# Optimization experiments

Hardware: AMD Instinct MI355X
Metric: run time of the kernel (lower is better)

## Reference

```python
import jax, jax.numpy as jnp
import numpy as np

BATCH, SEQ = 2, 4096
IN_FEATURES = 4096
OUT_FEATURES = 4096
BLOCK = 64                      # oft_block_size (bs)
RANK = IN_FEATURES // BLOCK     # number of diagonal blocks (r)


def setup_inputs() -> dict:
    key = jax.random.key(0)
    k1, k2, k3, k4 = jax.random.split(key, 4)
    x = jax.random.normal(k1, (BATCH, SEQ, IN_FEATURES), dtype=jnp.float32)
    # OFT adapter parameters: one (bs x bs) generator per block
    oft_r = jax.random.normal(k2, (RANK, BLOCK, BLOCK), dtype=jnp.float32) * 0.02
    # Dequantized GPTQ weight (out_features x in_features) + bias
    W = jax.random.normal(k3, (OUT_FEATURES, IN_FEATURES), dtype=jnp.float32) * 0.02
    b = jax.random.normal(k4, (OUT_FEATURES,), dtype=jnp.float32)
    return {"x": x, "oft_r": oft_r, "W": W, "b": b}


def _cayley_batch(data):
    # data: [r, bs, bs].  Q = (I - skew) @ (I + skew)^{-1}  (torch.linalg.solve left=False)
    bs = data.shape[-1]
    skew = 0.5 * (data - jnp.swapaxes(data, -1, -2))
    I = jnp.eye(bs, dtype=data.dtype)
    A = I + skew   # [r, bs, bs]
    B = I - skew
    # Solve Q A = B  ->  A^T Q^T = B^T
    Qt = jnp.linalg.solve(jnp.swapaxes(A, -1, -2), jnp.swapaxes(B, -1, -2))
    return jnp.swapaxes(Qt, -1, -2)


def reference(x, oft_r, W, b):
    rank, bs, _ = oft_r.shape
    # oft_rotation starts as identity; single active adapter -> rotation = Cayley(oft_r)
    oft_rotation = _cayley_batch(oft_r)            # [rank, bs, bs]
    batch_dims = x.shape[:-1]
    x_reshaped = x.reshape(*batch_dims, rank, bs)  # [..., r, k]
    x_rot = jnp.einsum('...rk,rkc->...rc', x_reshaped, oft_rotation)
    x_rot = x_rot.reshape(*batch_dims, rank * bs)  # [..., in_features]
    # quant_linear_module (dequantized): y = x_rot @ W^T + b
    return jnp.einsum('bsi,oi->bso', x_rot, W) + b
```

## Files before the change

kernel.cpp:

```cpp
#include <hip/hip_runtime.h>
#include <hip/hip_bf16.h>
#include <stdint.h>


typedef __bf16 bf16;
typedef __attribute__((ext_vector_type(4))) __bf16 bf16x4;
typedef __attribute__((ext_vector_type(8))) __bf16 bf16x8;
typedef __attribute__((ext_vector_type(4))) float f32x4;

__device__ __forceinline__ bf16 f2bf(float f) {
  unsigned u = __builtin_bit_cast(unsigned, f);
  u += 0x7fffu + ((u >> 16) & 1u);
  unsigned short h = (unsigned short)(u >> 16);
  return __builtin_bit_cast(bf16, h);
}

__global__ __launch_bounds__(256) void cayley_kernel(const float* __restrict__ oft_r,
                                                     float* __restrict__ Qxt) {
  __shared__ float St[64][68];
  __shared__ float Ta[64][65];
  __shared__ float Tb[64][65];
  const int tid = threadIdx.x;
  const int r = blockIdx.x;
  const float* D = oft_r + (size_t)r * 4096;

  for (int idx = tid; idx < 4096; idx += 256) {
    int i = idx >> 6, j = idx & 63;
    float s = 0.5f * (D[i * 64 + j] - D[j * 64 + i]);
    St[j][i] = s;
    Ta[i][j] = (i == j ? 1.0f : 0.0f) - s;
  }
  __syncthreads();

  const int j = tid & 63;
  const int w = tid >> 6;
  float (*Tin)[65] = Ta;
  float (*Tout)[65] = Tb;

  for (int it = 0; it < 5; ++it) {
    float out[16];
#pragma unroll
    for (int m = 0; m < 16; ++m) out[m] = ((w * 16 + m) == j ? 1.0f : 0.0f);
    for (int c = 0; c < 64; ++c) {
      float tc = Tin[c][j];
      f32x4 s0 = *reinterpret_cast<const f32x4*>(&St[c][w * 16]);
      f32x4 s1 = *reinterpret_cast<const f32x4*>(&St[c][w * 16 + 4]);
      f32x4 s2 = *reinterpret_cast<const f32x4*>(&St[c][w * 16 + 8]);
      f32x4 s3 = *reinterpret_cast<const f32x4*>(&St[c][w * 16 + 12]);
#pragma unroll
      for (int q = 0; q < 4; ++q) {
        out[q]      -= s0[q] * tc;
        out[4 + q]  -= s1[q] * tc;
        out[8 + q]  -= s2[q] * tc;
        out[12 + q] -= s3[q] * tc;
      }
    }
#pragma unroll
    for (int m = 0; m < 16; ++m) Tout[w * 16 + m][j] = out[m];
    __syncthreads();
    float (*tmp)[65] = Tin; Tin = Tout; Tout = tmp;
  }
  {
    float out[16];
#pragma unroll
    for (int m = 0; m < 16; ++m) out[m] = Tin[w * 16 + m][j];
    for (int c = 0; c < 64; ++c) {
      float tc = Tin[c][j];
      f32x4 s0 = *reinterpret_cast<const f32x4*>(&St[c][w * 16]);
      f32x4 s1 = *reinterpret_cast<const f32x4*>(&St[c][w * 16 + 4]);
      f32x4 s2 = *reinterpret_cast<const f32x4*>(&St[c][w * 16 + 8]);
      f32x4 s3 = *reinterpret_cast<const f32x4*>(&St[c][w * 16 + 12]);
#pragma unroll
      for (int q = 0; q < 4; ++q) {
        out[q]      -= s0[q] * tc;
        out[4 + q]  -= s1[q] * tc;
        out[8 + q]  -= s2[q] * tc;
        out[12 + q] -= s3[q] * tc;
      }
    }
#pragma unroll
    for (int m = 0; m < 16; ++m) Qxt[(size_t)r * 4096 + (w * 16 + m) * 64 + j] = out[m];
  }
}

__global__ __launch_bounds__(256) void foldcast_kernel(const float* __restrict__ W,
                                                       const float* __restrict__ Qxt,
                                                       bf16* __restrict__ Wp,
                                                       const float* __restrict__ x,
                                                       bf16* __restrict__ xb, long n) {
  __shared__ bf16 Wb[128 * 64];
  __shared__ bf16 Xt[64 * 64];
  const int tid = threadIdx.x;

  if (blockIdx.x >= 2048) {
    long i0 = ((long)(blockIdx.x - 2048) * 256 + tid) * 8;
    long stride = (long)(gridDim.x - 2048) * 256 * 8;
    for (long i = i0; i < n; i += stride) {
      f32x4 a = *reinterpret_cast<const f32x4*>(x + i);
      f32x4 b = *reinterpret_cast<const f32x4*>(x + i + 4);
      bf16x8 o;
      o[0] = f2bf(a[0]); o[1] = f2bf(a[1]); o[2] = f2bf(a[2]); o[3] = f2bf(a[3]);
      o[4] = f2bf(b[0]); o[5] = f2bf(b[1]); o[6] = f2bf(b[2]); o[7] = f2bf(b[3]);
      *reinterpret_cast<bf16x8*>(xb + i) = o;
    }
    return;
  }

  const int lane = tid & 63;
  const int wave = tid >> 6;
  const int o0 = (blockIdx.x & 31) * 128;
  const int r = blockIdx.x >> 5;
  const int fr = lane & 15;
  const int kg = lane >> 4;

#pragma unroll
  for (int i = 0; i < 8; ++i) {
    int c = i * 256 + tid;
    int row = c >> 4, c4 = c & 15;
    f32x4 v = *reinterpret_cast<const f32x4*>(W + (size_t)(o0 + row) * 4096 + r * 64 + c4 * 4);
    bf16x4 o; o[0] = f2bf(v[0]); o[1] = f2bf(v[1]); o[2] = f2bf(v[2]); o[3] = f2bf(v[3]);
    *reinterpret_cast<bf16x4*>(&Wb[row * 64 + c4 * 4]) = o;
  }
#pragma unroll
  for (int i = 0; i < 4; ++i) {
    int c = i * 256 + tid;
    int row = c >> 4, c4 = c & 15;
    f32x4 v = *reinterpret_cast<const f32x4*>(Qxt + (size_t)r * 4096 + row * 64 + c4 * 4);
    bf16x4 o; o[0] = f2bf(v[0]); o[1] = f2bf(v[1]); o[2] = f2bf(v[2]); o[3] = f2bf(v[3]);
    *reinterpret_cast<bf16x4*>(&Xt[row * 64 + c4 * 4]) = o;
  }
  __syncthreads();

  const int wm = wave * 32;
  f32x4 acc[2][4];
#pragma unroll
  for (int mi = 0; mi < 2; ++mi)
#pragma unroll
    for (int ni = 0; ni < 4; ++ni) acc[mi][ni] = (f32x4){0.f, 0.f, 0.f, 0.f};

#pragma unroll
  for (int kk = 0; kk < 64; kk += 32) {
    bf16x8 af[2], bx[4];
#pragma unroll
    for (int mi = 0; mi < 2; ++mi)
      af[mi] = *reinterpret_cast<const bf16x8*>(&Wb[(wm + mi * 16 + fr) * 64 + kk + kg * 8]);
#pragma unroll
    for (int ni = 0; ni < 4; ++ni)
      bx[ni] = *reinterpret_cast<const bf16x8*>(&Xt[(ni * 16 + fr) * 64 + kk + kg * 8]);
#pragma unroll
    for (int mi = 0; mi < 2; ++mi)
#pragma unroll
      for (int ni = 0; ni < 4; ++ni)
        acc[mi][ni] = __builtin_amdgcn_mfma_f32_16x16x32_bf16(af[mi], bx[ni], acc[mi][ni], 0, 0, 0);
  }

#pragma unroll
  for (int mi = 0; mi < 2; ++mi)
#pragma unroll
    for (int ni = 0; ni < 4; ++ni)
#pragma unroll
      for (int q = 0; q < 4; ++q) {
        int row = o0 + wm + mi * 16 + kg * 4 + q;
        int col = ni * 16 + fr;
        Wp[(size_t)row * 4096 + r * 64 + col] = f2bf(acc[mi][ni][q]);
      }
}


#define GLDS16(g, l) __builtin_amdgcn_global_load_lds( \
    (const __attribute__((address_space(1))) unsigned int*)(g), \
    (__attribute__((address_space(3))) unsigned int*)(l), 16, 0, 0)

#define VMCNT12 asm volatile("s_waitcnt vmcnt(12)" ::: "memory")
#define VMCNT8  asm volatile("s_waitcnt vmcnt(8)" ::: "memory")
#define VMCNT4  asm volatile("s_waitcnt vmcnt(4)" ::: "memory")
#define VMCNT0  asm volatile("s_waitcnt vmcnt(0)" ::: "memory")
#define NOWAIT  do {} while (0)
#define BARRIER() do { asm volatile("" ::: "memory"); \
  __builtin_amdgcn_s_barrier(); asm volatile("" ::: "memory"); } while (0)

#define MFMA16(AF, BF, RB) \
  _Pragma("unroll") \
  for (int m_ = 0; m_ < 4; ++m_) \
    _Pragma("unroll") \
    for (int n_ = 0; n_ < 4; ++n_) \
      acc[RB + m_][n_] = __builtin_amdgcn_mfma_f32_16x16x32_bf16(AF[m_], BF[n_], acc[RB + m_][n_], 0, 0, 0);

#define DO_T(S0, S1, SA, SB, TN, PRE, W2, W1) do { \
     \
    _Pragma("unroll") for (int n_ = 0; n_ < 4; ++n_) Ob[n_] = LDB(S0, n_); \
    _Pragma("unroll") for (int m_ = 0; m_ < 4; ++m_) Oa[m_] = LDA(S0, m_); \
    if (PRE) STG_A(TN, SA, 0); \
    BARRIER(); \
    __builtin_amdgcn_s_setprio(1); MFMA16(Oa, Ob, 0) __builtin_amdgcn_s_setprio(0); \
     \
    _Pragma("unroll") for (int m_ = 0; m_ < 4; ++m_) Ea[m_] = LDA(S0, 4 + m_); \
    if (PRE) STG_B(TN, SA, 0); \
    W2; \
    BARRIER(); \
    __builtin_amdgcn_s_setprio(1); MFMA16(Ea, Ob, 4) __builtin_amdgcn_s_setprio(0); \
     \
    _Pragma("unroll") for (int n_ = 0; n_ < 4; ++n_) Eb[n_] = LDB(S1, n_); \
    _Pragma("unroll") for (int m_ = 0; m_ < 4; ++m_) Oa[m_] = LDA(S1, m_); \
    if (PRE) STG_A(TN, SB, 1); \
    BARRIER(); \
    __builtin_amdgcn_s_setprio(1); MFMA16(Oa, Eb, 0) __builtin_amdgcn_s_setprio(0); \
     \
    _Pragma("unroll") for (int m_ = 0; m_ < 4; ++m_) Ea[m_] = LDA(S1, 4 + m_); \
    if (PRE) STG_B(TN, SB, 1); \
    W1; \
    BARRIER(); \
    __builtin_amdgcn_s_setprio(1); MFMA16(Ea, Eb, 4) __builtin_amdgcn_s_setprio(0); \
  } while (0)

__global__ __launch_bounds__(512, 2) void gemm_kernel(const bf16* __restrict__ A,
                                                      const bf16* __restrict__ B,
                                                      const float* __restrict__ bias,
                                                      float* __restrict__ C,
                                                      int M, int N, int K) {
  __shared__ bf16 lds[81920];
  const int tid = threadIdx.x;
  const int lane = tid & 63;
  const int wave = tid >> 6;
  const int wr = wave >> 2;
  const int wc = wave & 3;
  const int fr = lane & 15;
  const int kg = lane >> 4;
  const int m0 = blockIdx.y * 256;
  const int n0 = blockIdx.x * 256;

  f32x4 acc[8][4];
#pragma unroll
  for (int m = 0; m < 8; ++m)
#pragma unroll
    for (int n = 0; n < 4; ++n) acc[m][n] = (f32x4){0.f, 0.f, 0.f, 0.f};

  auto STG = [&](const bf16* src, int base_row, int t, int ks, int ldsbase) {
#pragma unroll
    for (int i = 0; i < 2; ++i) {
      int c = i * 512 + tid;
      int row = c >> 2, cc = c & 3;
      const bf16* g = src + (size_t)(base_row + row) * K + t * 64 + ks * 32
                      + ((cc ^ ((row >> 1) & 3)) << 3);
      GLDS16(g, &lds[ldsbase + ((i * 512 + wave * 64) << 3)]);
    }
  };
  auto STG_A = [&](int t, int slot, int ks) { STG(A, m0, t, ks, slot * 16384); };
  auto STG_B = [&](int t, int slot, int ks) { STG(B, n0, t, ks, slot * 16384 + 8192); };

  auto LDA = [&](int slot, int mi) -> bf16x8 {
    int row = wr * 128 + mi * 16 + fr;
    return *reinterpret_cast<const bf16x8*>(
        &lds[slot * 16384 + row * 32 + ((kg ^ ((row >> 1) & 3)) << 3)]);
  };
  auto LDB = [&](int slot, int ni) -> bf16x8 {
    int row = wc * 64 + ni * 16 + fr;
    return *reinterpret_cast<const bf16x8*>(
        &lds[slot * 16384 + 8192 + row * 32 + ((kg ^ ((row >> 1) & 3)) << 3)]);
  };

  STG_A(0, 0, 0); STG_B(0, 0, 0); STG_A(0, 1, 1); STG_B(0, 1, 1);
  STG_A(1, 2, 0); STG_B(1, 2, 0); STG_A(1, 3, 1); STG_B(1, 3, 1);
  VMCNT12;
  BARRIER();

  bf16x8 Oa[4], Ob[4], Ea[4], Eb[4];
  for (int t = 0; t < 60; t += 5) {
    DO_T(0, 1, 4, 0, t + 2, true, VMCNT12, VMCNT12);
    DO_T(2, 3, 1, 2, t + 3, true, VMCNT12, VMCNT12);
    DO_T(4, 0, 3, 4, t + 4, true, VMCNT12, VMCNT12);
    DO_T(1, 2, 0, 1, t + 5, true, VMCNT12, VMCNT12);
    DO_T(3, 4, 2, 3, t + 6, true, VMCNT12, VMCNT12);
  }
  DO_T(0, 1, 4, 0, 62, true,  VMCNT12, VMCNT12);
  DO_T(2, 3, 1, 2, 63, true,  VMCNT12, VMCNT12);
  DO_T(4, 0, 0, 0, 0,  false, VMCNT8,  VMCNT4);
  DO_T(1, 2, 0, 0, 0,  false, VMCNT0,  NOWAIT);

#pragma unroll
  for (int n = 0; n < 4; ++n) {
    int col = n0 + wc * 64 + n * 16 + fr;
    float bv = bias[col];
#pragma unroll
    for (int m = 0; m < 8; ++m) {
      int row0 = m0 + wr * 128 + m * 16 + kg * 4;
#pragma unroll
      for (int q = 0; q < 4; ++q)
        C[(size_t)(row0 + q) * N + col] = acc[m][n][q] + bv;
    }
  }
}

extern "C" void kernel_launch(void* const* d_in, const int* in_sizes, int n_in,
                              void* d_out, int out_size, void* d_ws, size_t ws_size,
                              hipStream_t stream) {
  const float* x     = (const float*)d_in[0];
  const float* oft_r = (const float*)d_in[1];
  const float* W     = (const float*)d_in[2];
  const float* b     = (const float*)d_in[3];
  float* y = (float*)d_out;

  char* ws = (char*)d_ws;
  float* Qxt = (float*)ws;
  bf16*  Wp  = (bf16*)(ws + (1u << 20));
  bf16*  xb  = (bf16*)(ws + (1u << 20) + (32u << 20));

  cayley_kernel<<<64, 256, 0, stream>>>(oft_r, Qxt);
  foldcast_kernel<<<4096, 256, 0, stream>>>(W, Qxt, Wp, x, xb, 33554432L);
  dim3 gg(4096 / 256, 8192 / 256);
  gemm_kernel<<<gg, 512, 0, stream>>>(xb, Wp, b, y, 8192, 4096, 4096);
}
```

Before: 323.0 us.

## Fuse Cayley solve and weight folding into one prep kernel

Merges the Cayley-transform kernel and the fold/cast kernel into one launch. Each of the first 64 blocks computes its rotation block in shared memory and keeps it in LDS as bf16, then loops over all 32 output chunks of W to fold it in. The remaining blocks cast x to bf16 at the same time. This removes a kernel launch and the fp32 Qxt round trip through global memory, and lets the x cast overlap the Cayley iterations. In exchange, all W folding is serialized onto only 64 blocks, each looping 32 times with barriers, which risks a long tail.

```diff
diff --git a/kernel.cpp b/kernel.cpp
--- a/kernel.cpp
+++ b/kernel.cpp
@@ -15,12 +15,34 @@
   return __builtin_bit_cast(bf16, h);
 }
 
-__global__ __launch_bounds__(256) void cayley_kernel(const float* __restrict__ oft_r,
-                                                     float* __restrict__ Qxt) {
-  __shared__ float St[64][68];
-  __shared__ float Ta[64][65];
-  __shared__ float Tb[64][65];
+__global__ __launch_bounds__(256) void prep_kernel(const float* __restrict__ oft_r,
+                                                   const float* __restrict__ W,
+                                                   bf16* __restrict__ Wp,
+                                                   const float* __restrict__ x,
+                                                   bf16* __restrict__ xb, long n) {
+  __shared__ char smem[50688];
   const int tid = threadIdx.x;
+
+  if (blockIdx.x >= 64) {
+    long i0 = ((long)(blockIdx.x - 64) * 256 + tid) * 8;
+    long stride = (long)(gridDim.x - 64) * 256 * 8;
+    for (long i = i0; i < n; i += stride) {
+      f32x4 a = *reinterpret_cast<const f32x4*>(x + i);
+      f32x4 b = *reinterpret_cast<const f32x4*>(x + i + 4);
+      bf16x8 o;
+      o[0] = f2bf(a[0]); o[1] = f2bf(a[1]); o[2] = f2bf(a[2]); o[3] = f2bf(a[3]);
+      o[4] = f2bf(b[0]); o[5] = f2bf(b[1]); o[6] = f2bf(b[2]); o[7] = f2bf(b[3]);
+      *reinterpret_cast<bf16x8*>(xb + i) = o;
+    }
+    return;
+  }
+
+  float (*St)[68] = reinterpret_cast<float(*)[68]>(smem);
+  float (*Ta)[65] = reinterpret_cast<float(*)[65]>(smem + 17408);
+  float (*Tb)[65] = reinterpret_cast<float(*)[65]>(smem + 34048);
+  bf16* Wb = reinterpret_cast<bf16*>(smem);
+  bf16* Xt = reinterpret_cast<bf16*>(smem + 17408);
+
   const int r = blockIdx.x;
   const float* D = oft_r + (size_t)r * 4096;
 
@@ -60,10 +82,11 @@
     __syncthreads();
     float (*tmp)[65] = Tin; Tin = Tout; Tout = tmp;
   }
+
+  float qout[16];
   {
-    float out[16];
-#pragma unroll
-    for (int m = 0; m < 16; ++m) out[m] = Tin[w * 16 + m][j];
+#pragma unroll
+    for (int m = 0; m < 16; ++m) qout[m] = Tin[w * 16 + m][j];
     for (int c = 0; c < 64; ++c) {
       float tc = Tin[c][j];
       f32x4 s0 = *reinterpret_cast<const f32x4*>(&St[c][w * 16]);
@@ -72,98 +95,70 @@
       f32x4 s3 = *reinterpret_cast<const f32x4*>(&St[c][w * 16 + 12]);
 #pragma unroll
       for (int q = 0; q < 4; ++q) {
-        out[q]      -= s0[q] * tc;
-        out[4 + q]  -= s1[q] * tc;
-        out[8 + q]  -= s2[q] * tc;
-        out[12 + q] -= s3[q] * tc;
+        qout[q]      -= s0[q] * tc;
+        qout[4 + q]  -= s1[q] * tc;
+        qout[8 + q]  -= s2[q] * tc;
+        qout[12 + q] -= s3[q] * tc;
       }
     }
-#pragma unroll
-    for (int m = 0; m < 16; ++m) Qxt[(size_t)r * 4096 + (w * 16 + m) * 64 + j] = out[m];
-  }
-}
-
-__global__ __launch_bounds__(256) void foldcast_kernel(const float* __restrict__ W,
-                                                       const float* __restrict__ Qxt,
-                                                       bf16* __restrict__ Wp,
-                                                       const float* __restrict__ x,
-                                                       bf16* __restrict__ xb, long n) {
-  __shared__ bf16 Wb[128 * 64];
-  __shared__ bf16 Xt[64 * 64];
-  const int tid = threadIdx.x;
-
-  if (blockIdx.x >= 2048) {
-    long i0 = ((long)(blockIdx.x - 2048) * 256 + tid) * 8;
-    long stride = (long)(gridDim.x - 2048) * 256 * 8;
-    for (long i = i0; i < n; i += stride) {
-      f32x4 a = *reinterpret_cast<const f32x4*>(x + i);
-      f32x4 b = *reinterpret_cast<const f32x4*>(x + i + 4);
-      bf16x8 o;
-      o[0] = f2bf(a[0]); o[1] = f2bf(a[1]); o[2] = f2bf(a[2]); o[3] = f2bf(a[3]);
-      o[4] = f2bf(b[0]); o[5] = f2bf(b[1]); o[6] = f2bf(b[2]); o[7] = f2bf(b[3]);
-      *reinterpret_cast<bf16x8*>(xb + i) = o;
-    }
-    return;
-  }
+  }
+  __syncthreads();
+
+#pragma unroll
+  for (int m = 0; m < 16; ++m) Xt[(w * 16 + m) * 64 + j] = f2bf(qout[m]);
 
   const int lane = tid & 63;
   const int wave = tid >> 6;
-  const int o0 = (blockIdx.x & 31) * 128;
-  const int r = blockIdx.x >> 5;
   const int fr = lane & 15;
   const int kg = lane >> 4;
-
-#pragma unroll
-  for (int i = 0; i < 8; ++i) {
-    int c = i * 256 + tid;
-    int row = c >> 4, c4 = c & 15;
-    f32x4 v = *reinterpret_cast<const f32x4*>(W + (size_t)(o0 + row) * 4096 + r * 64 + c4 * 4);
-    bf16x4 o; o[0] = f2bf(v[0]); o[1] = f2bf(v[1]); o[2] = f2bf(v[2]); o[3] = f2bf(v[3]);
-    *reinterpret_cast<bf16x4*>(&Wb[row * 64 + c4 * 4]) = o;
-  }
-#pragma unroll
-  for (int i = 0; i < 4; ++i) {
-    int c = i * 256 + tid;
-    int row = c >> 4, c4 = c & 15;
-    f32x4 v = *reinterpret_cast<const f32x4*>(Qxt + (size_t)r * 4096 + row * 64 + c4 * 4);
-    bf16x4 o; o[0] = f2bf(v[0]); o[1] = f2bf(v[1]); o[2] = f2bf(v[2]); o[3] = f2bf(v[3]);
-    *reinterpret_cast<bf16x4*>(&Xt[row * 64 + c4 * 4]) = o;
-  }
-  __syncthreads();
-
   const int wm = wave * 32;
-  f32x4 acc[2][4];
-#pragma unroll
-  for (int mi = 0; mi < 2; ++mi)
-#pragma unroll
-    for (int ni = 0; ni < 4; ++ni) acc[mi][ni] = (f32x4){0.f, 0.f, 0.f, 0.f};
-
-#pragma unroll
-  for (int kk = 0; kk < 64; kk += 32) {
-    bf16x8 af[2], bx[4];
+
+  for (int oc = 0; oc < 32; ++oc) {
+    const int o0 = oc * 128;
+#pragma unroll
+    for (int i = 0; i < 8; ++i) {
+      int c = i * 256 + tid;
+      int row = c >> 4, c4 = c & 15;
+      f32x4 v = *reinterpret_cast<const f32x4*>(W + (size_t)(o0 + row) * 4096 + r * 64 + c4 * 4);
+      bf16x4 o; o[0] = f2bf(v[0]); o[1] = f2bf(v[1]); o[2] = f2bf(v[2]); o[3] = f2bf(v[3]);
+      *reinterpret_cast<bf16x4*>(&Wb[row * 64 + c4 * 4]) = o;
+    }
+    __syncthreads();
+
+    f32x4 acc[2][4];
 #pragma unroll
     for (int mi = 0; mi < 2; ++mi)
-      af[mi] = *reinterpret_cast<const bf16x8*>(&Wb[(wm + mi * 16 + fr) * 64 + kk + kg * 8]);
-#pragma unroll
-    for (int ni = 0; ni < 4; ++ni)
-      bx[ni] = *reinterpret_cast<const bf16x8*>(&Xt[(ni * 16 + fr) * 64 + kk + kg * 8]);
+#pragma unroll
+      for (int ni = 0; ni < 4; ++ni) acc[mi][ni] = (f32x4){0.f, 0.f, 0.f, 0.f};
+
+#pragma unroll
+    for (int kk = 0; kk < 64; kk += 32) {
+      bf16x8 af[2], bx[4];
+#pragma unroll
+      for (int mi = 0; mi < 2; ++mi)
+        af[mi] = *reinterpret_cast<const bf16x8*>(&Wb[(wm + mi * 16 + fr) * 64 + kk + kg * 8]);
+#pragma unroll
+      for (int ni = 0; ni < 4; ++ni)
+        bx[ni] = *reinterpret_cast<const bf16x8*>(&Xt[(ni * 16 + fr) * 64 + kk + kg * 8]);
+#pragma unroll
+      for (int mi = 0; mi < 2; ++mi)
+#pragma unroll
+        for (int ni = 0; ni < 4; ++ni)
+          acc[mi][ni] = __builtin_amdgcn_mfma_f32_16x16x32_bf16(af[mi], bx[ni], acc[mi][ni], 0, 0, 0);
+    }
+
 #pragma unroll
     for (int mi = 0; mi < 2; ++mi)
 #pragma unroll
       for (int ni = 0; ni < 4; ++ni)
-        acc[mi][ni] = __builtin_amdgcn_mfma_f32_16x16x32_bf16(af[mi], bx[ni], acc[mi][ni], 0, 0, 0);
-  }
-
-#pragma unroll
-  for (int mi = 0; mi < 2; ++mi)
-#pragma unroll
-    for (int ni = 0; ni < 4; ++ni)
-#pragma unroll
-      for (int q = 0; q < 4; ++q) {
-        int row = o0 + wm + mi * 16 + kg * 4 + q;
-        int col = ni * 16 + fr;
-        Wp[(size_t)row * 4096 + r * 64 + col] = f2bf(acc[mi][ni][q]);
-      }
+#pragma unroll
+        for (int q = 0; q < 4; ++q) {
+          int row = o0 + wm + mi * 16 + kg * 4 + q;
+          int col = ni * 16 + fr;
+          Wp[(size_t)row * 4096 + r * 64 + col] = f2bf(acc[mi][ni][q]);
+        }
+    __syncthreads();
+  }
 }
 
 
@@ -301,12 +296,10 @@
   float* y = (float*)d_out;
 
   char* ws = (char*)d_ws;
-  float* Qxt = (float*)ws;
-  bf16*  Wp  = (bf16*)(ws + (1u << 20));
-  bf16*  xb  = (bf16*)(ws + (1u << 20) + (32u << 20));
-
-  cayley_kernel<<<64, 256, 0, stream>>>(oft_r, Qxt);
-  foldcast_kernel<<<4096, 256, 0, stream>>>(W, Qxt, Wp, x, xb, 33554432L);
+  bf16* Wp = (bf16*)ws;
+  bf16* xb = (bf16*)(ws + (32u << 20));
+
+  prep_kernel<<<2112, 256, 0, stream>>>(oft_r, W, Wp, x, xb, 33554432L);
   dim3 gg(4096 / 256, 8192 / 256);
   gemm_kernel<<<gg, 512, 0, stream>>>(xb, Wp, b, y, 8192, 4096, 4096);
 }
```

Result: slower. 340.8 us (+5.5%).
